# Kernel tuning notes

Hardware: AMD Instinct MI355X
Metric: run time of the kernel (lower is better)

The kernel has to match this reference:

```python
import jax, jax.numpy as jnp
import numpy as np

B, N, L = 2, 2048, 2048
DQ, DKV, H, WF = 1024, 1024, 16, 4
HD = DQ // H
EPS = 1e-5


def _ln(x, g, b):
    m = jnp.mean(x, axis=-1, keepdims=True)
    v = jnp.mean(jnp.square(x - m), axis=-1, keepdims=True)
    return (x - m) * jax.lax.rsqrt(v + EPS) * g + b


def setup_inputs() -> dict:
    key = jax.random.key(0)
    ks = jax.random.split(key, 12)
    s = 0.02
    return {
        "x_q": jax.random.normal(ks[0], (B, N, DQ), jnp.float32),
        "x_kv": jax.random.normal(ks[1], (B, L, DKV), jnp.float32),
        "qn_g": jnp.ones((DQ,), jnp.float32),
        "qn_b": jnp.zeros((DQ,), jnp.float32),
        "kvn_g": jnp.ones((DKV,), jnp.float32),
        "kvn_b": jnp.zeros((DKV,), jnp.float32),
        "Wq": jax.random.normal(ks[2], (DQ, DQ), jnp.float32) * s,
        "bq": jnp.zeros((DQ,), jnp.float32),
        "Wk": jax.random.normal(ks[3], (DQ, DKV), jnp.float32) * s,
        "bk": jnp.zeros((DQ,), jnp.float32),
        "Wv": jax.random.normal(ks[4], (DQ, DKV), jnp.float32) * s,
        "bv": jnp.zeros((DQ,), jnp.float32),
        "Wo": jax.random.normal(ks[5], (DQ, DQ), jnp.float32) * s,
        "bo": jnp.zeros((DQ,), jnp.float32),
        "n2_g": jnp.ones((DQ,), jnp.float32),
        "n2_b": jnp.zeros((DQ,), jnp.float32),
        "W1": jax.random.normal(ks[6], (WF * DQ, DQ), jnp.float32) * s,
        "b1": jnp.zeros((WF * DQ,), jnp.float32),
        "W2": jax.random.normal(ks[7], (DQ, WF * DQ), jnp.float32) * s,
        "b2": jnp.zeros((DQ,), jnp.float32),
    }


def reference(x_q, x_kv, qn_g, qn_b, kvn_g, kvn_b, Wq, bq, Wk, bk, Wv, bv,
              Wo, bo, n2_g, n2_b, W1, b1, W2, b2):
    # projections (torch Linear: x @ W.T + b)
    q = (_ln(x_q, qn_g, qn_b) @ Wq.T + bq).reshape(B, N, H, HD)
    kvn = _ln(x_kv, kvn_g, kvn_b)
    k = (kvn @ Wk.T + bk).reshape(B, L, H, HD)
    v = (kvn @ Wv.T + bv).reshape(B, L, H, HD)

    # attention with softmax-1: exp(s)/(1 + sum exp(s)), numerically stable
    scale = 1.0 / jnp.sqrt(jnp.float32(HD))
    s = jnp.einsum("bnhd,blhd->bhnl", q, k) * scale  # [B,H,N,L]
    m = jnp.max(s, axis=-1, keepdims=True)
    m = jnp.maximum(m, 0.0)  # include the implicit zero logit of softmax-1
    p = jnp.exp(s - m)
    denom = jnp.sum(p, axis=-1, keepdims=True) + jnp.exp(-m)
    attn = p / denom
    attn_out = jnp.einsum("bhnl,blhd->bnhd", attn, v).reshape(B, N, DQ)

    # residual + out proj
    x = x_q + (attn_out @ Wo.T + bo)
    # residual MLP (GELU, exact/erf as torch nn.GELU default)
    h = jax.nn.gelu(_ln(x, n2_g, n2_b) @ W1.T + b1, approximate=False)
    x = x + (h @ W2.T + b2)
    return x
```

## Files before the change

kernel.cpp:

```cpp
#include <hip/hip_runtime.h>
#include <hip/hip_bf16.h>
#include <stdint.h>

#define DEV __device__ __forceinline__

typedef unsigned short ushort_t;
typedef __attribute__((ext_vector_type(8))) short bf16x8;
typedef __attribute__((ext_vector_type(4))) float f32x4;

DEV uint32_t f2bf2(float lo, float hi) {
  uint32_t d;
  asm("v_cvt_pk_bf16_f32 %0, %1, %2" : "=v"(d) : "v"(lo), "v"(hi));
  return d;
}
DEV ushort_t f2bf(float f) { return (ushort_t)f2bf2(f, f); }

DEV void gload_lds16(const void* gp, void* lp) {
  __builtin_amdgcn_global_load_lds(
      (__attribute__((address_space(1))) void*)(void*)(uintptr_t)gp,
      (__attribute__((address_space(3))) void*)lp, 16, 0, 0);
}

__global__ __launch_bounds__(256) void cvt_all(
    const float* __restrict__ Wq, const float* __restrict__ Wk,
    const float* __restrict__ Wv, const float* __restrict__ Wo,
    const float* __restrict__ W1, const float* __restrict__ W2,
    ushort_t* __restrict__ WQKVB, ushort_t* __restrict__ WoB,
    ushort_t* __restrict__ W1B, ushort_t* __restrict__ W2B) {
  int i = blockIdx.x * 256 + threadIdx.x;
  const float* src; ushort_t* dst; int j;
  if (i < 262144)            { src = Wq; dst = WQKVB;            j = i; }
  else if (i < 524288)       { src = Wk; dst = WQKVB + 1048576;  j = i - 262144; }
  else if (i < 786432)       { src = Wv; dst = WQKVB + 2097152;  j = i - 524288; }
  else if (i < 1048576)      { src = Wo; dst = WoB;              j = i - 786432; }
  else if (i < 2097152)      { src = W1; dst = W1B;              j = i - 1048576; }
  else                       { src = W2; dst = W2B;              j = i - 2097152; }
  float4 v = ((const float4*)src)[j];
  uint2 o; o.x = f2bf2(v.x, v.y); o.y = f2bf2(v.z, v.w);
  ((uint2*)dst)[j] = o;
}

DEV void ln_row(const float* __restrict__ x, const float* __restrict__ g,
                const float* __restrict__ be, ushort_t* __restrict__ out, int row) {
  const int t = threadIdx.x;
  const float4 v = ((const float4*)(x + (size_t)row * 1024))[t];
  float s = v.x + v.y + v.z + v.w;
  float sq = v.x * v.x + v.y * v.y + v.z * v.z + v.w * v.w;
#pragma unroll
  for (int d = 1; d < 64; d <<= 1) { s += __shfl_xor(s, d); sq += __shfl_xor(sq, d); }
  __shared__ float sm[8];
  const int w = t >> 6, lane = t & 63;
  if (lane == 0) { sm[w * 2] = s; sm[w * 2 + 1] = sq; }
  __syncthreads();
  s = sm[0] + sm[2] + sm[4] + sm[6];
  sq = sm[1] + sm[3] + sm[5] + sm[7];
  const float mean = s * (1.f / 1024.f);
  const float var = sq * (1.f / 1024.f) - mean * mean;
  const float rstd = rsqrtf(var + 1e-5f);
  const float4 gv = ((const float4*)g)[t];
  const float4 bv = ((const float4*)be)[t];
  uint2 o;
  o.x = f2bf2((v.x - mean) * rstd * gv.x + bv.x, (v.y - mean) * rstd * gv.y + bv.y);
  o.y = f2bf2((v.z - mean) * rstd * gv.z + bv.z, (v.w - mean) * rstd * gv.w + bv.w);
  ((uint2*)(out + (size_t)row * 1024))[t] = o;
}

__global__ __launch_bounds__(256) void ln_bf16(const float* __restrict__ x,
                                               const float* __restrict__ g,
                                               const float* __restrict__ be,
                                               ushort_t* __restrict__ out) {
  ln_row(x, g, be, out, blockIdx.x);
}

__global__ __launch_bounds__(256) void ln_fused(
    const float* __restrict__ x_q, const float* __restrict__ x_kv,
    const float* __restrict__ qg, const float* __restrict__ qb,
    const float* __restrict__ kg, const float* __restrict__ kb,
    ushort_t* __restrict__ oq, ushort_t* __restrict__ okv) {
  const int r = blockIdx.x;
  if (r < 4096) ln_row(x_q, qg, qb, oq, r);
  else ln_row(x_kv, kg, kb, okv, r - 4096);
}

DEV void xcd_remap(int gx, int gy, int& bx, int& by) {
  const int lin = by * gx + bx;
  const int xcd = lin & 7, s = lin >> 3;
  by = xcd * (gy >> 3) + s / gx;
  bx = s % gx;
}

enum { EPI_BF16 = 0, EPI_KV = 1, EPI_RESID = 2, EPI_GELU = 3, EPI_QKV = 4 };

template <int BM, int TN, int BK, int EPI>
__global__ __launch_bounds__(256, (BM == 64) ? 4 : 3) void gemm_bt(
    const ushort_t* __restrict__ A,
    const ushort_t* __restrict__ A2,
    const ushort_t* __restrict__ Wb,
    const float* __restrict__ bias, const float* __restrict__ bias2,
    const float* __restrict__ bias3,
    const float* __restrict__ resid,
    void* __restrict__ outp, void* __restrict__ outp2, void* __restrict__ outp3,
    int M, int N, int K, float oscale) {
  constexpr int WAVES_N = (TN == 128 || BM == 64) ? 2 : 1;
  constexpr int WAVES_M = 4 / WAVES_N;
  constexpr int NI = BM / WAVES_M / 16;
  constexpr int NJ = TN / WAVES_N / 16;
  constexpr int CH = BK / 8;
  constexpr int NA = (BM * CH) / 256;
  constexpr int NBL = (TN * CH) / 256;
  constexpr int KS = BK / 32;
  __shared__ ushort_t As[2][BM * BK];
  __shared__ ushort_t Bs[2][TN * BK];
  const int t = threadIdx.x;
  const int w = t >> 6, lane = t & 63;
  const int qd = lane >> 4, ql = lane & 15;
  int bx = blockIdx.x, by = blockIdx.y;
  xcd_remap(gridDim.x, gridDim.y, bx, by);
  const int m0 = by * BM, n0 = bx * TN;
  const int wm = (w / WAVES_N) * (BM / WAVES_M);
  const int wn = (w % WAVES_N) * (TN / WAVES_N);
  const int sw = (BK == 64) ? (ql & 7) : ((ql >> 1) & 3);

  const ushort_t* Ause = (EPI == EPI_QKV && n0 >= 1024) ? A2 : A;

  const ushort_t* pa[NA];
#pragma unroll
  for (int p = 0; p < NA; p++) {
    int n = p * 256 + t, row = n / CH, c = n % CH;
    int g = (BK == 64) ? (c ^ (row & 7)) : (c ^ ((row >> 1) & 3));
    pa[p] = Ause + (size_t)(m0 + row) * K + g * 8;
  }
  const ushort_t* pb[NBL];
#pragma unroll
  for (int p = 0; p < NBL; p++) {
    int n = p * 256 + t, row = n / CH, c = n % CH;
    int g = (BK == 64) ? (c ^ (row & 7)) : (c ^ ((row >> 1) & 3));
    pb[p] = Wb + (size_t)(n0 + row) * K + g * 8;
  }

#pragma unroll
  for (int p = 0; p < NA; p++) { gload_lds16(pa[p], &As[0][(p * 256 + t) * 8]); pa[p] += BK; }
#pragma unroll
  for (int p = 0; p < NBL; p++) { gload_lds16(pb[p], &Bs[0][(p * 256 + t) * 8]); pb[p] += BK; }
  __syncthreads();

  f32x4 acc[NI][NJ] = {};
  const int NIT = K / BK;
  int cur = 0;

  for (int it = 0; it < NIT; ++it) {
    if (it + 1 < NIT) {
#pragma unroll
      for (int p = 0; p < NA; p++) { gload_lds16(pa[p], &As[1 ^ cur][(p * 256 + t) * 8]); pa[p] += BK; }
#pragma unroll
      for (int p = 0; p < NBL; p++) { gload_lds16(pb[p], &Bs[1 ^ cur][(p * 256 + t) * 8]); pb[p] += BK; }
    }
    const ushort_t* Ac = As[cur];
    const ushort_t* Bc = Bs[cur];
#pragma unroll
    for (int ks = 0; ks < KS; ks++) {
      bf16x8 af[NI], bf[NJ];
#pragma unroll
      for (int i = 0; i < NI; i++)
        af[i] = *(const bf16x8*)&Ac[(wm + i * 16 + ql) * BK + ((ks * 4 + qd) ^ sw) * 8];
#pragma unroll
      for (int j = 0; j < NJ; j++)
        bf[j] = *(const bf16x8*)&Bc[(wn + j * 16 + ql) * BK + ((ks * 4 + qd) ^ sw) * 8];
#pragma unroll
      for (int i = 0; i < NI; i++)
#pragma unroll
        for (int j = 0; j < NJ; j++)
          acc[i][j] = __builtin_amdgcn_mfma_f32_16x16x32_bf16(af[i], bf[j], acc[i][j], 0, 0, 0);
    }
    __syncthreads();
    cur ^= 1;
  }

#pragma unroll
  for (int i = 0; i < NI; i++) {
    const int mr = m0 + wm + i * 16 + qd * 4;
#pragma unroll
    for (int j = 0; j < NJ; j++) {
      const int col = n0 + wn + j * 16 + ql;
      f32x4 v = acc[i][j];
      if constexpr (EPI == EPI_BF16) {
        const float bb = bias[col];
        ushort_t* o = (ushort_t*)outp;
#pragma unroll
        for (int r = 0; r < 4; r++) o[(size_t)(mr + r) * N + col] = f2bf((v[r] + bb) * oscale);
      } else if constexpr (EPI == EPI_QKV) {
        if (col < 1024) {
          const float bb = bias[col];
          ushort_t* o = (ushort_t*)outp;
#pragma unroll
          for (int r = 0; r < 4; r++) o[(size_t)(mr + r) * 1024 + col] = f2bf((v[r] + bb) * oscale);
        } else if (col < 2048) {
          const int c2 = col - 1024;
          const float bb = bias2[c2];
          ushort_t* o = (ushort_t*)outp2;
#pragma unroll
          for (int r = 0; r < 4; r++) o[(size_t)(mr + r) * 1024 + c2] = f2bf(v[r] + bb);
        } else {
          const int vc = col - 2048;
          const float bb = bias3[vc];
          const int h = vc >> 6, d = vc & 63;
          const int b = mr >> 11, l0 = mr & 2047;
          uint2 pk;
          pk.x = f2bf2(v[0] + bb, v[1] + bb);
          pk.y = f2bf2(v[2] + bb, v[3] + bb);
          *(uint2*)((ushort_t*)outp3 + ((((size_t)b * 16 + h) * 64 + d) * 2048 + l0)) = pk;
        }
      } else if constexpr (EPI == EPI_RESID) {
        const float bb = bias[col];
        float* o = (float*)outp;
#pragma unroll
        for (int r = 0; r < 4; r++) {
          size_t idx = (size_t)(mr + r) * N + col;
          o[idx] = resid[idx] + v[r] + bb;
        }
      } else if constexpr (EPI == EPI_GELU) {
        const float bb = bias[col];
        ushort_t* o = (ushort_t*)outp;
#pragma unroll
        for (int r = 0; r < 4; r++) {
          float x = v[r] + bb;
          float gx = 0.5f * x * (1.0f + erff(x * 0.70710678118654752f));
          o[(size_t)(mr + r) * N + col] = f2bf(gx);
        }
      }
    }
  }
}

__global__ __launch_bounds__(256, 2) void flash_attn(const ushort_t* __restrict__ Qg,
                                                     const ushort_t* __restrict__ Kg,
                                                     const ushort_t* __restrict__ VTg,
                                                     ushort_t* __restrict__ Og) {
  __shared__ ushort_t QPs[128 * 64];
  __shared__ ushort_t Ks[2][64 * 64];
  __shared__ ushort_t Vs[2][64 * 64];
  const int t = threadIdx.x, w = t >> 6, lane = t & 63;
  const int qd = lane >> 4, ql = lane & 15;
  int bx = blockIdx.x, bh = blockIdx.y;
  xcd_remap(gridDim.x, gridDim.y, bx, bh);
  const int b = bh >> 4, h = bh & 15;
  const int n0 = bx * 128;
  const ushort_t* Qp = Qg + ((size_t)b * 2048 + n0) * 1024 + h * 64;
  const ushort_t* Kp = Kg + (size_t)b * 2048 * 1024 + h * 64;
  const ushort_t* Vp = VTg + (size_t)bh * 64 * 2048;
  const int sw = ql & 7;

  const ushort_t* kp2[2];
  const ushort_t* vp2[2];
#pragma unroll
  for (int p = 0; p < 2; p++) {
    int n = p * 256 + t, row = n >> 3, c = (n & 7) ^ (row & 7);
    kp2[p] = Kp + (size_t)row * 1024 + c * 8;
    vp2[p] = Vp + (size_t)row * 2048 + c * 8;
  }

#pragma unroll
  for (int p = 0; p < 4; p++) {
    int n = p * 256 + t, row = n >> 3, c = (n & 7) ^ (row & 7);
    gload_lds16(Qp + (size_t)row * 1024 + c * 8, &QPs[n * 8]);
  }
#pragma unroll
  for (int p = 0; p < 2; p++) {
    int n = p * 256 + t;
    gload_lds16(kp2[p], &Ks[0][n * 8]);
    gload_lds16(vp2[p], &Vs[0][n * 8]);
    kp2[p] += 64 * 1024;
    vp2[p] += 64;
  }
  __syncthreads();

  bf16x8 aq[2][2];
#pragma unroll
  for (int i = 0; i < 2; i++)
#pragma unroll
    for (int ks = 0; ks < 2; ks++)
      aq[i][ks] = *(const bf16x8*)&QPs[(w * 32 + i * 16 + ql) * 64 + ((ks * 4 + qd) ^ sw) * 8];
  __syncthreads();

  f32x4 accO[2][4] = {};
  float lro2[2] = {0.f, 0.f};

  int cur = 0;
  for (int lt = 0; lt < 32; ++lt) {
    if (lt + 1 < 32) {
#pragma unroll
      for (int p = 0; p < 2; p++) {
        int n = p * 256 + t;
        gload_lds16(kp2[p], &Ks[1 ^ cur][n * 8]);
        gload_lds16(vp2[p], &Vs[1 ^ cur][n * 8]);
        kp2[p] += 64 * 1024;
        vp2[p] += 64;
      }
    }
    const ushort_t* Kc = Ks[cur];
    const ushort_t* Vc = Vs[cur];

    f32x4 accS[4][2] = {};
#pragma unroll
    for (int ks = 0; ks < 2; ks++) {
      bf16x8 bk[4];
#pragma unroll
      for (int j = 0; j < 4; j++)
        bk[j] = *(const bf16x8*)&Kc[(j * 16 + ql) * 64 + ((ks * 4 + qd) ^ sw) * 8];
#pragma unroll
      for (int j = 0; j < 4; j++)
#pragma unroll
        for (int i = 0; i < 2; i++)
          accS[j][i] = __builtin_amdgcn_mfma_f32_16x16x32_bf16(bk[j], aq[i][ks], accS[j][i], 0, 0, 0);
    }

#pragma unroll
    for (int j = 0; j < 4; j++)
#pragma unroll
      for (int i = 0; i < 2; i++) {
        f32x4 p;
#pragma unroll
        for (int r = 0; r < 4; r++) {
          p[r] = __builtin_amdgcn_exp2f(accS[j][i][r]);
          lro2[i] += p[r];
        }
        const int n = w * 32 + i * 16 + ql;
        const int coff = (((j * 2 + (qd >> 1)) ^ sw) << 3) + ((qd & 1) << 2);
        uint2 pk; pk.x = f2bf2(p[0], p[1]); pk.y = f2bf2(p[2], p[3]);
        *(uint2*)&QPs[n * 64 + coff] = pk;
      }

#pragma unroll
    for (int ks = 0; ks < 2; ks++) {
      bf16x8 ap[2], bv[4];
#pragma unroll
      for (int i = 0; i < 2; i++)
        ap[i] = *(const bf16x8*)&QPs[(w * 32 + i * 16 + ql) * 64 + ((ks * 4 + qd) ^ sw) * 8];
#pragma unroll
      for (int jo = 0; jo < 4; jo++)
        bv[jo] = *(const bf16x8*)&Vc[(jo * 16 + ql) * 64 + ((ks * 4 + qd) ^ sw) * 8];
#pragma unroll
      for (int i = 0; i < 2; i++)
#pragma unroll
        for (int jo = 0; jo < 4; jo++)
          accO[i][jo] = __builtin_amdgcn_mfma_f32_16x16x32_bf16(ap[i], bv[jo], accO[i][jo], 0, 0, 0);
    }

    __syncthreads();
    cur ^= 1;
  }

  float dn[2];
#pragma unroll
  for (int i = 0; i < 2; i++) {
    float l = lro2[i];
    l += __shfl_xor(l, 16);
    l += __shfl_xor(l, 32);
    dn[i] = l + 1.0f;
  }

#pragma unroll
  for (int i = 0; i < 2; i++)
#pragma unroll
    for (int r = 0; r < 4; r++) {
      const float inv = 1.0f / __shfl(dn[i], qd * 4 + r);
      const int row = n0 + w * 32 + i * 16 + qd * 4 + r;
#pragma unroll
      for (int jo = 0; jo < 4; jo++)
        Og[((size_t)b * 2048 + row) * 1024 + h * 64 + jo * 16 + ql] =
            f2bf(accO[i][jo][r] * inv);
    }
}

extern "C" void kernel_launch(void* const* d_in, const int* in_sizes, int n_in,
                              void* d_out, int out_size, void* d_ws, size_t ws_size,
                              hipStream_t stream) {
  const float* x_q = (const float*)d_in[0];
  const float* x_kv = (const float*)d_in[1];
  const float* qn_g = (const float*)d_in[2];
  const float* qn_b = (const float*)d_in[3];
  const float* kvn_g = (const float*)d_in[4];
  const float* kvn_b = (const float*)d_in[5];
  const float* Wq = (const float*)d_in[6];
  const float* bq = (const float*)d_in[7];
  const float* Wk = (const float*)d_in[8];
  const float* bk = (const float*)d_in[9];
  const float* Wv = (const float*)d_in[10];
  const float* bv = (const float*)d_in[11];
  const float* Wo = (const float*)d_in[12];
  const float* bo = (const float*)d_in[13];
  const float* n2_g = (const float*)d_in[14];
  const float* n2_b = (const float*)d_in[15];
  const float* W1 = (const float*)d_in[16];
  const float* b1 = (const float*)d_in[17];
  const float* W2 = (const float*)d_in[18];
  const float* b2 = (const float*)d_in[19];

  char* ws = (char*)d_ws;
  const size_t MB = 1ull << 20;
  ushort_t* WQKVB = (ushort_t*)(ws + 0 * MB);
  ushort_t* WoB = (ushort_t*)(ws + 6 * MB);
  ushort_t* W1B = (ushort_t*)(ws + 8 * MB);
  ushort_t* W2B = (ushort_t*)(ws + 16 * MB);
  ushort_t* LNQ = (ushort_t*)(ws + 24 * MB);
  ushort_t* LNKV = (ushort_t*)(ws + 32 * MB);
  ushort_t* Qb = (ushort_t*)(ws + 40 * MB);
  ushort_t* Kb = (ushort_t*)(ws + 48 * MB);
  ushort_t* VTb = (ushort_t*)(ws + 56 * MB);
  ushort_t* AOb = (ushort_t*)(ws + 64 * MB);
  float* Xf = (float*)(ws + 72 * MB);
  ushort_t* LN2 = (ushort_t*)(ws + 88 * MB);
  ushort_t* Hb = (ushort_t*)(ws + 24 * MB);

  const float QSCALE = 0.18033688011112042f;

  cvt_all<<<12288, 256, 0, stream>>>(Wq, Wk, Wv, Wo, W1, W2, WQKVB, WoB, W1B, W2B);
  ln_fused<<<8192, 256, 0, stream>>>(x_q, x_kv, qn_g, qn_b, kvn_g, kvn_b, LNQ, LNKV);

  gemm_bt<128, 128, 32, EPI_QKV><<<dim3(24, 32), 256, 0, stream>>>(
      LNQ, LNKV, WQKVB, bq, bk, bv, nullptr, Qb, Kb, VTb, 4096, 3072, 1024, QSCALE);

  flash_attn<<<dim3(16, 32), 256, 0, stream>>>(Qb, Kb, VTb, AOb);

  gemm_bt<64, 64, 64, EPI_RESID><<<dim3(16, 64), 256, 0, stream>>>(
      AOb, nullptr, WoB, bo, nullptr, nullptr, x_q, Xf, nullptr, nullptr,
      4096, 1024, 1024, 1.0f);
  ln_bf16<<<4096, 256, 0, stream>>>(Xf, n2_g, n2_b, LN2);
  gemm_bt<128, 128, 32, EPI_GELU><<<dim3(32, 32), 256, 0, stream>>>(
      LN2, nullptr, W1B, b1, nullptr, nullptr, nullptr, Hb, nullptr, nullptr,
      4096, 4096, 1024, 1.0f);
  gemm_bt<64, 64, 64, EPI_RESID><<<dim3(16, 64), 256, 0, stream>>>(
      Hb, nullptr, W2B, b2, nullptr, nullptr, Xf, (float*)d_out, nullptr, nullptr,
      4096, 1024, 4096, 1.0f);
}
```

Baseline: 361.1 us.

## Merge weight convert with layernorm, use polynomial GELU, raise MFMA priority

Folds the weight fp32-to-bf16 conversion and the two input layernorms into a single kernel launch, removing one launch and the gap between them. Replaces the libm erff in the GELU epilogue with an Abramowitz-Stegun polynomial built on hardware rcp and exp2, which cuts the cost of the epilogue at a small accuracy cost. Wraps the attention MFMA blocks in s_setprio to favour the matrix-issuing waves.

```diff
diff --git a/kernel.cpp b/kernel.cpp
--- a/kernel.cpp
+++ b/kernel.cpp
@@ -21,23 +21,18 @@
       (__attribute__((address_space(3))) void*)lp, 16, 0, 0);
 }
 
-__global__ __launch_bounds__(256) void cvt_all(
-    const float* __restrict__ Wq, const float* __restrict__ Wk,
-    const float* __restrict__ Wv, const float* __restrict__ Wo,
-    const float* __restrict__ W1, const float* __restrict__ W2,
-    ushort_t* __restrict__ WQKVB, ushort_t* __restrict__ WoB,
-    ushort_t* __restrict__ W1B, ushort_t* __restrict__ W2B) {
-  int i = blockIdx.x * 256 + threadIdx.x;
-  const float* src; ushort_t* dst; int j;
-  if (i < 262144)            { src = Wq; dst = WQKVB;            j = i; }
-  else if (i < 524288)       { src = Wk; dst = WQKVB + 1048576;  j = i - 262144; }
-  else if (i < 786432)       { src = Wv; dst = WQKVB + 2097152;  j = i - 524288; }
-  else if (i < 1048576)      { src = Wo; dst = WoB;              j = i - 786432; }
-  else if (i < 2097152)      { src = W1; dst = W1B;              j = i - 1048576; }
-  else                       { src = W2; dst = W2B;              j = i - 2097152; }
-  float4 v = ((const float4*)src)[j];
-  uint2 o; o.x = f2bf2(v.x, v.y); o.y = f2bf2(v.z, v.w);
-  ((uint2*)dst)[j] = o;
+DEV float gelu_fast(float x) {
+  const float z = fabsf(x) * 0.70710678118654752f;
+  const float t = __builtin_amdgcn_rcpf(fmaf(0.3275911f, z, 1.0f));
+  float p = fmaf(1.061405429f, t, -1.453152027f);
+  p = fmaf(p, t, 1.421413741f);
+  p = fmaf(p, t, -0.284496736f);
+  p = fmaf(p, t, 0.254829592f);
+  p *= t;
+  const float e = __builtin_amdgcn_exp2f(z * z * -1.4426950408889634f);
+  const float er = fmaf(-p, e, 1.0f);
+  const float s = copysignf(er, x);
+  return 0.5f * x * (1.0f + s);
 }
 
 DEV void ln_row(const float* __restrict__ x, const float* __restrict__ g,
@@ -65,21 +60,40 @@
   ((uint2*)(out + (size_t)row * 1024))[t] = o;
 }
 
+__global__ __launch_bounds__(256) void cvt_ln(
+    const float* __restrict__ Wq, const float* __restrict__ Wk,
+    const float* __restrict__ Wv, const float* __restrict__ Wo,
+    const float* __restrict__ W1, const float* __restrict__ W2,
+    ushort_t* __restrict__ WQKVB, ushort_t* __restrict__ WoB,
+    ushort_t* __restrict__ W1B, ushort_t* __restrict__ W2B,
+    const float* __restrict__ x_q, const float* __restrict__ x_kv,
+    const float* __restrict__ qg, const float* __restrict__ qb,
+    const float* __restrict__ kg, const float* __restrict__ kb,
+    ushort_t* __restrict__ oq, ushort_t* __restrict__ okv) {
+  if (blockIdx.x < 12288) {
+    int i = blockIdx.x * 256 + threadIdx.x;
+    const float* src; ushort_t* dst; int j;
+    if (i < 262144)            { src = Wq; dst = WQKVB;            j = i; }
+    else if (i < 524288)       { src = Wk; dst = WQKVB + 1048576;  j = i - 262144; }
+    else if (i < 786432)       { src = Wv; dst = WQKVB + 2097152;  j = i - 524288; }
+    else if (i < 1048576)      { src = Wo; dst = WoB;              j = i - 786432; }
+    else if (i < 2097152)      { src = W1; dst = W1B;              j = i - 1048576; }
+    else                       { src = W2; dst = W2B;              j = i - 2097152; }
+    float4 v = ((const float4*)src)[j];
+    uint2 o; o.x = f2bf2(v.x, v.y); o.y = f2bf2(v.z, v.w);
+    ((uint2*)dst)[j] = o;
+  } else {
+    const int r = blockIdx.x - 12288;
+    if (r < 4096) ln_row(x_q, qg, qb, oq, r);
+    else ln_row(x_kv, kg, kb, okv, r - 4096);
+  }
+}
+
 __global__ __launch_bounds__(256) void ln_bf16(const float* __restrict__ x,
                                                const float* __restrict__ g,
                                                const float* __restrict__ be,
                                                ushort_t* __restrict__ out) {
   ln_row(x, g, be, out, blockIdx.x);
-}
-
-__global__ __launch_bounds__(256) void ln_fused(
-    const float* __restrict__ x_q, const float* __restrict__ x_kv,
-    const float* __restrict__ qg, const float* __restrict__ qb,
-    const float* __restrict__ kg, const float* __restrict__ kb,
-    ushort_t* __restrict__ oq, ushort_t* __restrict__ okv) {
-  const int r = blockIdx.x;
-  if (r < 4096) ln_row(x_q, qg, qb, oq, r);
-  else ln_row(x_kv, kg, kb, okv, r - 4096);
 }
 
 DEV void xcd_remap(int gx, int gy, int& bx, int& by) {
@@ -222,11 +236,8 @@
         const float bb = bias[col];
         ushort_t* o = (ushort_t*)outp;
 #pragma unroll
-        for (int r = 0; r < 4; r++) {
-          float x = v[r] + bb;
-          float gx = 0.5f * x * (1.0f + erff(x * 0.70710678118654752f));
-          o[(size_t)(mr + r) * N + col] = f2bf(gx);
-        }
+        for (int r = 0; r < 4; r++)
+          o[(size_t)(mr + r) * N + col] = f2bf(gelu_fast(v[r] + bb));
       }
     }
   }
@@ -307,11 +318,13 @@
 #pragma unroll
       for (int j = 0; j < 4; j++)
         bk[j] = *(const bf16x8*)&Kc[(j * 16 + ql) * 64 + ((ks * 4 + qd) ^ sw) * 8];
+      __builtin_amdgcn_s_setprio(1);
 #pragma unroll
       for (int j = 0; j < 4; j++)
 #pragma unroll
         for (int i = 0; i < 2; i++)
           accS[j][i] = __builtin_amdgcn_mfma_f32_16x16x32_bf16(bk[j], aq[i][ks], accS[j][i], 0, 0, 0);
+      __builtin_amdgcn_s_setprio(0);
     }
 
 #pragma unroll
@@ -339,11 +352,13 @@
 #pragma unroll
       for (int jo = 0; jo < 4; jo++)
         bv[jo] = *(const bf16x8*)&Vc[(jo * 16 + ql) * 64 + ((ks * 4 + qd) ^ sw) * 8];
+      __builtin_amdgcn_s_setprio(1);
 #pragma unroll
       for (int i = 0; i < 2; i++)
 #pragma unroll
         for (int jo = 0; jo < 4; jo++)
           accO[i][jo] = __builtin_amdgcn_mfma_f32_16x16x32_bf16(ap[i], bv[jo], accO[i][jo], 0, 0, 0);
+      __builtin_amdgcn_s_setprio(0);
     }
 
     __syncthreads();
@@ -414,8 +429,8 @@
 
   const float QSCALE = 0.18033688011112042f;
 
-  cvt_all<<<12288, 256, 0, stream>>>(Wq, Wk, Wv, Wo, W1, W2, WQKVB, WoB, W1B, W2B);
-  ln_fused<<<8192, 256, 0, stream>>>(x_q, x_kv, qn_g, qn_b, kvn_g, kvn_b, LNQ, LNKV);
+  cvt_ln<<<20480, 256, 0, stream>>>(Wq, Wk, Wv, Wo, W1, W2, WQKVB, WoB, W1B, W2B,
+                                    x_q, x_kv, qn_g, qn_b, kvn_g, kvn_b, LNQ, LNKV);
 
   gemm_bt<128, 128, 32, EPI_QKV><<<dim3(24, 32), 256, 0, stream>>>(
       LNQ, LNKV, WQKVB, bq, bk, bv, nullptr, Qb, Kb, VTb, 4096, 3072, 1024, QSCALE);
```

Measured after the change: 354.8 us. About the same (-1.8%).
